# Kernel tuning notes

Hardware: AMD Instinct MI355X
Metric: run time of the kernel (lower is better)

## Reference

```python
import jax, jax.numpy as jnp
import numpy as np

WS = 7          # window_size
NH = 4          # num_heads
C = 128         # channels
N = WS * WS     # tokens per window = 49
BW = 4096       # number of windows total (batch * windows_per_image)
NW = 64         # windows per image (mask leading dim)


def _rel_pos_index(ws):
    coords = np.stack(np.meshgrid(np.arange(ws), np.arange(ws), indexing='ij'))
    cf = coords.reshape(2, -1)
    rel = (cf[:, :, None] - cf[:, None, :]).transpose(1, 2, 0)
    rel[:, :, 0] += ws - 1
    rel[:, :, 1] += ws - 1
    rel[:, :, 0] *= 2 * ws - 1
    return jnp.asarray(rel.sum(-1).ravel(), dtype=jnp.int32)  # [N*N]


def setup_inputs() -> dict:
    key = jax.random.key(0)
    ks = jax.random.split(key, 6)
    x = jax.random.normal(ks[0], (BW, N, C), dtype=jnp.float32)
    qkv_w = jax.random.normal(ks[1], (C, 3 * C), dtype=jnp.float32) * 0.02
    qkv_b = jnp.zeros((3 * C,), dtype=jnp.float32)
    proj_w = jax.random.normal(ks[2], (C, C), dtype=jnp.float32) * 0.02
    proj_b = jnp.zeros((C,), dtype=jnp.float32)
    bias_table = jax.random.normal(ks[3], ((2 * WS - 1) ** 2, NH), dtype=jnp.float32) * 0.02
    # Swin shifted-window mask: 0 where attention allowed, -100 where blocked
    keep = jax.random.bernoulli(ks[4], 0.5, (NW, N, N))
    mask = jnp.where(keep, 0.0, -100.0).astype(jnp.float32)
    return {"x": x, "qkv_w": qkv_w, "qkv_b": qkv_b, "proj_w": proj_w,
            "proj_b": proj_b, "bias_table": bias_table, "mask": mask}


def reference(x, qkv_w, qkv_b, proj_w, proj_b, bias_table, mask):
    B_, n, c = x.shape
    h = NH
    d = c // h
    scale = d ** -0.5

    qkv = x @ qkv_w + qkv_b                       # [B_, N, 3C]
    qkv = qkv.reshape(B_, n, 3, h, d).transpose(2, 0, 3, 1, 4)  # [3, B_, h, N, d]
    q, k, v = qkv[0], qkv[1], qkv[2]

    attn = jnp.einsum('bhnd,bhmd->bhnm', q * scale, k)          # [B_, h, N, N]

    idx = _rel_pos_index(WS)
    rpb = bias_table[idx].reshape(n, n, h).transpose(2, 0, 1)   # [h, N, N]
    attn = attn + rpb[None]

    nW = mask.shape[0]
    attn = attn.reshape(-1, nW, h, n, n) + mask[None, :, None]  # [B, nW, h, N, N]
    attn = attn.reshape(-1, h, n, n)
    attn = jax.nn.softmax(attn, axis=-1)

    out = jnp.einsum('bhnm,bhmd->bhnd', attn, v)  # [B_, h, N, d]
    out = out.transpose(0, 2, 1, 3).reshape(B_, n, c)
    return out @ proj_w + proj_b
```

## Files before the change

### kernel.cpp

```cpp
#include <hip/hip_runtime.h>

#define NTOK 49
#define CH   128
#define NHEAD 4
#define SCALE 0.17677669529663687f

typedef __bf16 bf16x8 __attribute__((ext_vector_type(8)));
typedef short  s16x8  __attribute__((ext_vector_type(8)));
typedef float  f32x4  __attribute__((ext_vector_type(4)));

__device__ __forceinline__ unsigned short f2bf(float f) {
  unsigned int u = __builtin_bit_cast(unsigned int, f);
  u += 0x7FFFu + ((u >> 16) & 1u);
  return (unsigned short)(u >> 16);
}

__device__ __forceinline__ f32x4 mfma_bf16(s16x8 a, s16x8 b, f32x4 c) {
  return __builtin_amdgcn_mfma_f32_16x16x32_bf16(
      __builtin_bit_cast(bf16x8, a), __builtin_bit_cast(bf16x8, b), c, 0, 0, 0);
}

__global__ void prep_kernel(const float* __restrict__ qkv_w,
                            const float* __restrict__ proj_w,
                            const float* __restrict__ bias_table,
                            unsigned short* __restrict__ wT,
                            unsigned short* __restrict__ pT,
                            float* __restrict__ rpb) {
  int t = blockIdx.x * 256 + threadIdx.x;
  if (t < 384 * 128) {
    int n = t >> 7, k = t & 127;
    float v = qkv_w[k * 384 + n];
    if (n < 128) v *= SCALE;
    wT[n * 128 + k] = f2bf(v);
  } else if (t < 384 * 128 + 128 * 128) {
    int u = t - 384 * 128;
    int n = u >> 7, k = u & 127;
    pT[n * 128 + k] = f2bf(proj_w[k * 128 + n]);
  } else if (t < 384 * 128 + 128 * 128 + NHEAD * NTOK * NTOK) {
    int u = t - (384 * 128 + 128 * 128);
    int h = u / (NTOK * NTOK);
    int ij = u % (NTOK * NTOK);
    int i = ij / NTOK, j = ij % NTOK;
    int idx = (i / 7 - j / 7 + 6) * 13 + (i % 7 - j % 7 + 6);
    rpb[h * (NTOK * NTOK) + ij] = bias_table[idx * NHEAD + h];
  }
}

__global__ __launch_bounds__(256, 2)
void attn_fused_kernel(const float* __restrict__ x,
                       const float* __restrict__ qkv_b,
                       const float* __restrict__ proj_b,
                       const float* __restrict__ mask,
                       const unsigned short* __restrict__ wT,
                       const unsigned short* __restrict__ pT,
                       const float* __restrict__ rpb,
                       float* __restrict__ out) {
  __shared__ __align__(16) char smem_raw[76800];
  unsigned short* const Xs     = (unsigned short*)smem_raw;
  unsigned short* const QKbase = (unsigned short*)(smem_raw + 17408);
  unsigned short* const VTbase = (unsigned short*)(smem_raw + 58368);

  const int w    = blockIdx.x;
  const int tid  = threadIdx.x;
  const int wave = tid >> 6;
  const int lane = tid & 63;
  const int quad = lane >> 4;
  const int l16  = lane & 15;
  const int h    = wave;

  unsigned short* const qs = QKbase + wave * 5120;
  unsigned short* const ks = qs + 2560;
  unsigned short* const ps = QKbase + wave * 5120;
  unsigned short* const vt = VTbase + wave * 2304;

  const f32x4 fzero = {0.f, 0.f, 0.f, 0.f};

  {
    const float* xw = x + (size_t)w * (NTOK * CH);
    for (int t = tid; t < NTOK * 32; t += 256) {
      const int row = t >> 5;
      const int c4  = (t & 31) << 2;
      const float4 v = *(const float4*)(xw + row * CH + c4);
      ushort4 pk;
      pk.x = f2bf(v.x); pk.y = f2bf(v.y); pk.z = f2bf(v.z); pk.w = f2bf(v.w);
      *(ushort4*)(Xs + row * 136 + c4) = pk;
    }
    for (int t = tid; t < 15 * 32; t += 256) {
      const int row = 49 + (t >> 5);
      const int c4  = (t & 31) << 2;
      ushort4 z; z.x = 0; z.y = 0; z.z = 0; z.w = 0;
      *(ushort4*)(Xs + row * 136 + c4) = z;
    }
  }
  __syncthreads();

#pragma unroll
  for (int part = 0; part < 3; ++part) {
    f32x4 acc[4][2];
#pragma unroll
    for (int mt = 0; mt < 4; ++mt)
#pragma unroll
      for (int nt = 0; nt < 2; ++nt) acc[mt][nt] = fzero;
    const int nbase = part * 128 + h * 32;
#pragma unroll
    for (int kt = 0; kt < 4; ++kt) {
      s16x8 a[4], b[2];
#pragma unroll
      for (int mt = 0; mt < 4; ++mt)
        a[mt] = *(const s16x8*)(Xs + (mt * 16 + l16) * 136 + kt * 32 + quad * 8);
#pragma unroll
      for (int nt = 0; nt < 2; ++nt)
        b[nt] = *(const s16x8*)(wT + (size_t)(nbase + nt * 16 + l16) * 128 + kt * 32 + quad * 8);
#pragma unroll
      for (int mt = 0; mt < 4; ++mt)
#pragma unroll
        for (int nt = 0; nt < 2; ++nt)
          acc[mt][nt] = mfma_bf16(a[mt], b[nt], acc[mt][nt]);
    }
#pragma unroll
    for (int nt = 0; nt < 2; ++nt) {
      float bias = qkv_b[nbase + nt * 16 + l16];
      if (part == 0) bias *= SCALE;
#pragma unroll
      for (int mt = 0; mt < 4; ++mt)
#pragma unroll
        for (int r = 0; r < 4; ++r) {
          const int row = mt * 16 + quad * 4 + r;
          const int col = nt * 16 + l16;
          const unsigned short bv = f2bf(acc[mt][nt][r] + bias);
          if (part == 0)      qs[row * 40 + col] = bv;
          else if (part == 1) ks[row * 40 + col] = bv;
          else                vt[col * 72 + row] = bv;
        }
    }
  }
  __syncthreads();

  s16x8 qf[4], kf[4];
#pragma unroll
  for (int mt = 0; mt < 4; ++mt)
    qf[mt] = *(const s16x8*)(qs + (mt * 16 + l16) * 40 + quad * 8);
#pragma unroll
  for (int nt = 0; nt < 4; ++nt)
    kf[nt] = *(const s16x8*)(ks + (nt * 16 + l16) * 40 + quad * 8);
  f32x4 s[4][4];
#pragma unroll
  for (int mt = 0; mt < 4; ++mt)
#pragma unroll
    for (int nt = 0; nt < 4; ++nt)
      s[mt][nt] = mfma_bf16(qf[mt], kf[nt], fzero);

  const float* maskw = mask + (size_t)(w & 63) * (NTOK * NTOK);
  const float* rpbh  = rpb + h * (NTOK * NTOK);
  float rinv[4][4];
#pragma unroll
  for (int mt = 0; mt < 4; ++mt) {
#pragma unroll
    for (int r = 0; r < 4; ++r) {
      const int i = mt * 16 + quad * 4 + r;
      float vals[4];
      float vmax = -1e30f;
#pragma unroll
      for (int nt = 0; nt < 4; ++nt) {
        const int j = nt * 16 + l16;
        float v = -1e30f;
        if (i < NTOK && j < NTOK) {
          const int ij = i * NTOK + j;
          v = s[mt][nt][r] + rpbh[ij] + maskw[ij];
        }
        vals[nt] = v;
        vmax = fmaxf(vmax, v);
      }
#pragma unroll
      for (int off = 1; off < 16; off <<= 1)
        vmax = fmaxf(vmax, __shfl_xor(vmax, off, 64));
      float rsum = 0.f;
#pragma unroll
      for (int nt = 0; nt < 4; ++nt) {
        const float e = __expf(vals[nt] - vmax);
        vals[nt] = e;
        rsum += e;
      }
#pragma unroll
      for (int off = 1; off < 16; off <<= 1)
        rsum += __shfl_xor(rsum, off, 64);
      rinv[mt][r] = 1.f / rsum;
#pragma unroll
      for (int nt = 0; nt < 4; ++nt)
        ps[i * 72 + nt * 16 + l16] = f2bf(vals[nt]);
    }
  }

  f32x4 o[4][2];
#pragma unroll
  for (int mt = 0; mt < 4; ++mt)
#pragma unroll
    for (int nt = 0; nt < 2; ++nt) o[mt][nt] = fzero;
#pragma unroll
  for (int kt = 0; kt < 2; ++kt) {
    s16x8 pf[4], vf[2];
#pragma unroll
    for (int mt = 0; mt < 4; ++mt)
      pf[mt] = *(const s16x8*)(ps + (mt * 16 + l16) * 72 + kt * 32 + quad * 8);
#pragma unroll
    for (int nt = 0; nt < 2; ++nt)
      vf[nt] = *(const s16x8*)(vt + (nt * 16 + l16) * 72 + kt * 32 + quad * 8);
#pragma unroll
    for (int mt = 0; mt < 4; ++mt)
#pragma unroll
      for (int nt = 0; nt < 2; ++nt)
        o[mt][nt] = mfma_bf16(pf[mt], vf[nt], o[mt][nt]);
  }

  unsigned short* const ao = Xs;
#pragma unroll
  for (int mt = 0; mt < 4; ++mt)
#pragma unroll
    for (int nt = 0; nt < 2; ++nt)
#pragma unroll
      for (int r = 0; r < 4; ++r) {
        const int row = mt * 16 + quad * 4 + r;
        const int col = h * 32 + nt * 16 + l16;
        ao[row * 136 + col] = f2bf(o[mt][nt][r] * rinv[mt][r]);
      }
  __syncthreads();

  f32x4 po[4][2];
#pragma unroll
  for (int mt = 0; mt < 4; ++mt)
#pragma unroll
    for (int nt = 0; nt < 2; ++nt) po[mt][nt] = fzero;
#pragma unroll
  for (int kt = 0; kt < 4; ++kt) {
    s16x8 a[4], b[2];
#pragma unroll
    for (int mt = 0; mt < 4; ++mt)
      a[mt] = *(const s16x8*)(ao + (mt * 16 + l16) * 136 + kt * 32 + quad * 8);
#pragma unroll
    for (int nt = 0; nt < 2; ++nt)
      b[nt] = *(const s16x8*)(pT + (size_t)(h * 32 + nt * 16 + l16) * 128 + kt * 32 + quad * 8);
#pragma unroll
    for (int mt = 0; mt < 4; ++mt)
#pragma unroll
      for (int nt = 0; nt < 2; ++nt)
        po[mt][nt] = mfma_bf16(a[mt], b[nt], po[mt][nt]);
  }
  float* outw = out + (size_t)w * (NTOK * CH);
#pragma unroll
  for (int nt = 0; nt < 2; ++nt) {
    const int col = h * 32 + nt * 16 + l16;
    const float pb = proj_b[col];
#pragma unroll
    for (int mt = 0; mt < 4; ++mt)
#pragma unroll
      for (int r = 0; r < 4; ++r) {
        const int row = mt * 16 + quad * 4 + r;
        if (row < NTOK) outw[row * CH + col] = po[mt][nt][r] + pb;
      }
  }
}

extern "C" void kernel_launch(void* const* d_in, const int* in_sizes, int n_in,
                              void* d_out, int out_size, void* d_ws, size_t ws_size,
                              hipStream_t stream) {
  (void)in_sizes; (void)n_in; (void)out_size; (void)ws_size;
  const float* x          = (const float*)d_in[0];
  const float* qkv_w      = (const float*)d_in[1];
  const float* qkv_b      = (const float*)d_in[2];
  const float* proj_w     = (const float*)d_in[3];
  const float* proj_b     = (const float*)d_in[4];
  const float* bias_table = (const float*)d_in[5];
  const float* mask       = (const float*)d_in[6];
  float* out = (float*)d_out;

  unsigned short* wT = (unsigned short*)d_ws;
  unsigned short* pT = wT + 384 * 128;
  float* rpb = (float*)(pT + 128 * 128);

  const int prep_items = 384 * 128 + 128 * 128 + NHEAD * NTOK * NTOK;
  prep_kernel<<<(prep_items + 255) / 256, 256, 0, stream>>>(qkv_w, proj_w, bias_table,
                                                            wT, pT, rpb);
  attn_fused_kernel<<<4096, 256, 0, stream>>>(x, qkv_b, proj_b, mask, wT, pT, rpb, out);
}
```

Before: 319.7 us.

## Split window rows across eight waves and compute softmax sums with MFMA

Doubles the block to 512 threads so each head's rows are split across two waves. This halves per-wave MFMA and register work and raises waves per CU under the fixed LDS budget. Softmax drops the max-subtraction and shuffle reductions: it stores exp(logit) directly and gets row sums with an MFMA against a ones vector. The prep kernel now reads weights coalesced. The risk is that unshifted exp can overflow for large logits, and an extra barrier is needed because P overwrites the Q/K buffers.

```diff
diff --git a/kernel.cpp b/kernel.cpp
--- a/kernel.cpp
+++ b/kernel.cpp
@@ -28,14 +28,14 @@
                             float* __restrict__ rpb) {
   int t = blockIdx.x * 256 + threadIdx.x;
   if (t < 384 * 128) {
-    int n = t >> 7, k = t & 127;
-    float v = qkv_w[k * 384 + n];
+    int k = t / 384, n = t % 384;
+    float v = qkv_w[t];
     if (n < 128) v *= SCALE;
     wT[n * 128 + k] = f2bf(v);
   } else if (t < 384 * 128 + 128 * 128) {
     int u = t - 384 * 128;
-    int n = u >> 7, k = u & 127;
-    pT[n * 128 + k] = f2bf(proj_w[k * 128 + n]);
+    int k = u >> 7, n = u & 127;
+    pT[n * 128 + k] = f2bf(proj_w[u]);
   } else if (t < 384 * 128 + 128 * 128 + NHEAD * NTOK * NTOK) {
     int u = t - (384 * 128 + 128 * 128);
     int h = u / (NTOK * NTOK);
@@ -46,7 +46,7 @@
   }
 }
 
-__global__ __launch_bounds__(256, 2)
+__global__ __launch_bounds__(512, 4)
 void attn_fused_kernel(const float* __restrict__ x,
                        const float* __restrict__ qkv_b,
                        const float* __restrict__ proj_b,
@@ -56,28 +56,30 @@
                        const float* __restrict__ rpb,
                        float* __restrict__ out) {
   __shared__ __align__(16) char smem_raw[76800];
-  unsigned short* const Xs     = (unsigned short*)smem_raw;
-  unsigned short* const QKbase = (unsigned short*)(smem_raw + 17408);
-  unsigned short* const VTbase = (unsigned short*)(smem_raw + 58368);
+  unsigned short* const Xs = (unsigned short*)smem_raw;
+  unsigned short* const QK = (unsigned short*)(smem_raw + 17408);
+  unsigned short* const VT = (unsigned short*)(smem_raw + 58368);
 
   const int w    = blockIdx.x;
   const int tid  = threadIdx.x;
-  const int wave = tid >> 6;
+  const int wv   = tid >> 6;
+  const int h    = wv & 3;
+  const int mh   = wv >> 2;
   const int lane = tid & 63;
   const int quad = lane >> 4;
   const int l16  = lane & 15;
-  const int h    = wave;
-
-  unsigned short* const qs = QKbase + wave * 5120;
+  const int rowbase = mh * 32;
+
+  unsigned short* const qs = QK + h * 5120;
   unsigned short* const ks = qs + 2560;
-  unsigned short* const ps = QKbase + wave * 5120;
-  unsigned short* const vt = VTbase + wave * 2304;
+  unsigned short* const ps = QK + h * 5120;
+  unsigned short* const vt = VT + h * 2304;
 
   const f32x4 fzero = {0.f, 0.f, 0.f, 0.f};
 
   {
     const float* xw = x + (size_t)w * (NTOK * CH);
-    for (int t = tid; t < NTOK * 32; t += 256) {
+    for (int t = tid; t < NTOK * 32; t += 512) {
       const int row = t >> 5;
       const int c4  = (t & 31) << 2;
       const float4 v = *(const float4*)(xw + row * CH + c4);
@@ -85,7 +87,7 @@
       pk.x = f2bf(v.x); pk.y = f2bf(v.y); pk.z = f2bf(v.z); pk.w = f2bf(v.w);
       *(ushort4*)(Xs + row * 136 + c4) = pk;
     }
-    for (int t = tid; t < 15 * 32; t += 256) {
+    for (int t = tid; t < 15 * 32; t += 512) {
       const int row = 49 + (t >> 5);
       const int c4  = (t & 31) << 2;
       ushort4 z; z.x = 0; z.y = 0; z.z = 0; z.w = 0;
@@ -94,72 +96,76 @@
   }
   __syncthreads();
 
-#pragma unroll
-  for (int part = 0; part < 3; ++part) {
-    f32x4 acc[4][2];
-#pragma unroll
-    for (int mt = 0; mt < 4; ++mt)
-#pragma unroll
-      for (int nt = 0; nt < 2; ++nt) acc[mt][nt] = fzero;
-    const int nbase = part * 128 + h * 32;
-#pragma unroll
-    for (int kt = 0; kt < 4; ++kt) {
-      s16x8 a[4], b[2];
-#pragma unroll
-      for (int mt = 0; mt < 4; ++mt)
-        a[mt] = *(const s16x8*)(Xs + (mt * 16 + l16) * 136 + kt * 32 + quad * 8);
-#pragma unroll
-      for (int nt = 0; nt < 2; ++nt)
-        b[nt] = *(const s16x8*)(wT + (size_t)(nbase + nt * 16 + l16) * 128 + kt * 32 + quad * 8);
-#pragma unroll
-      for (int mt = 0; mt < 4; ++mt)
+  f32x4 acc[3][2][2];
+#pragma unroll
+  for (int p = 0; p < 3; ++p)
+#pragma unroll
+    for (int mt = 0; mt < 2; ++mt)
+#pragma unroll
+      for (int nt = 0; nt < 2; ++nt) acc[p][mt][nt] = fzero;
+
+#pragma unroll
+  for (int kt = 0; kt < 4; ++kt) {
+    s16x8 a[2];
+#pragma unroll
+    for (int mt = 0; mt < 2; ++mt)
+      a[mt] = *(const s16x8*)(Xs + (rowbase + mt * 16 + l16) * 136 + kt * 32 + quad * 8);
+#pragma unroll
+    for (int p = 0; p < 3; ++p) {
+      s16x8 b[2];
+#pragma unroll
+      for (int nt = 0; nt < 2; ++nt)
+        b[nt] = *(const s16x8*)(wT + (size_t)(p * 128 + h * 32 + nt * 16 + l16) * 128 +
+                                kt * 32 + quad * 8);
+#pragma unroll
+      for (int mt = 0; mt < 2; ++mt)
 #pragma unroll
         for (int nt = 0; nt < 2; ++nt)
-          acc[mt][nt] = mfma_bf16(a[mt], b[nt], acc[mt][nt]);
-    }
+          acc[p][mt][nt] = mfma_bf16(a[mt], b[nt], acc[p][mt][nt]);
+    }
+  }
+#pragma unroll
+  for (int p = 0; p < 3; ++p)
 #pragma unroll
     for (int nt = 0; nt < 2; ++nt) {
-      float bias = qkv_b[nbase + nt * 16 + l16];
-      if (part == 0) bias *= SCALE;
-#pragma unroll
-      for (int mt = 0; mt < 4; ++mt)
+      const int col = nt * 16 + l16;
+      float bias = qkv_b[p * 128 + h * 32 + col];
+      if (p == 0) bias *= SCALE;
+#pragma unroll
+      for (int mt = 0; mt < 2; ++mt)
 #pragma unroll
         for (int r = 0; r < 4; ++r) {
-          const int row = mt * 16 + quad * 4 + r;
-          const int col = nt * 16 + l16;
-          const unsigned short bv = f2bf(acc[mt][nt][r] + bias);
-          if (part == 0)      qs[row * 40 + col] = bv;
-          else if (part == 1) ks[row * 40 + col] = bv;
-          else                vt[col * 72 + row] = bv;
+          const int row = rowbase + mt * 16 + quad * 4 + r;
+          const unsigned short bv = f2bf(acc[p][mt][nt][r] + bias);
+          if (p == 0)      qs[row * 40 + col] = bv;
+          else if (p == 1) ks[row * 40 + col] = bv;
+          else             vt[col * 72 + row] = bv;
         }
     }
-  }
-  __syncthreads();
-
-  s16x8 qf[4], kf[4];
-#pragma unroll
-  for (int mt = 0; mt < 4; ++mt)
-    qf[mt] = *(const s16x8*)(qs + (mt * 16 + l16) * 40 + quad * 8);
+  __syncthreads();
+
+  s16x8 qf[2], kf[4];
+#pragma unroll
+  for (int mt = 0; mt < 2; ++mt)
+    qf[mt] = *(const s16x8*)(qs + (rowbase + mt * 16 + l16) * 40 + quad * 8);
 #pragma unroll
   for (int nt = 0; nt < 4; ++nt)
     kf[nt] = *(const s16x8*)(ks + (nt * 16 + l16) * 40 + quad * 8);
-  f32x4 s[4][4];
-#pragma unroll
-  for (int mt = 0; mt < 4; ++mt)
+  f32x4 s[2][4];
+#pragma unroll
+  for (int mt = 0; mt < 2; ++mt)
 #pragma unroll
     for (int nt = 0; nt < 4; ++nt)
       s[mt][nt] = mfma_bf16(qf[mt], kf[nt], fzero);
+  __syncthreads();
 
   const float* maskw = mask + (size_t)(w & 63) * (NTOK * NTOK);
   const float* rpbh  = rpb + h * (NTOK * NTOK);
-  float rinv[4][4];
-#pragma unroll
-  for (int mt = 0; mt < 4; ++mt) {
+#pragma unroll
+  for (int mt = 0; mt < 2; ++mt)
 #pragma unroll
     for (int r = 0; r < 4; ++r) {
-      const int i = mt * 16 + quad * 4 + r;
-      float vals[4];
-      float vmax = -1e30f;
+      const int i = rowbase + mt * 16 + quad * 4 + r;
 #pragma unroll
       for (int nt = 0; nt < 4; ++nt) {
         const int j = nt * 16 + l16;
@@ -168,79 +174,71 @@
           const int ij = i * NTOK + j;
           v = s[mt][nt][r] + rpbh[ij] + maskw[ij];
         }
-        vals[nt] = v;
-        vmax = fmaxf(vmax, v);
+        ps[i * 72 + j] = f2bf(__expf(v));
       }
-#pragma unroll
-      for (int off = 1; off < 16; off <<= 1)
-        vmax = fmaxf(vmax, __shfl_xor(vmax, off, 64));
-      float rsum = 0.f;
-#pragma unroll
-      for (int nt = 0; nt < 4; ++nt) {
-        const float e = __expf(vals[nt] - vmax);
-        vals[nt] = e;
-        rsum += e;
-      }
-#pragma unroll
-      for (int off = 1; off < 16; off <<= 1)
-        rsum += __shfl_xor(rsum, off, 64);
-      rinv[mt][r] = 1.f / rsum;
-#pragma unroll
-      for (int nt = 0; nt < 4; ++nt)
-        ps[i * 72 + nt * 16 + l16] = f2bf(vals[nt]);
-    }
-  }
-
-  f32x4 o[4][2];
-#pragma unroll
-  for (int mt = 0; mt < 4; ++mt)
+    }
+
+  s16x8 pf[2][2], vf[2][2], ones;
+#pragma unroll
+  for (int e = 0; e < 8; ++e) ones[e] = (short)0x3F80;
+#pragma unroll
+  for (int mt = 0; mt < 2; ++mt)
+#pragma unroll
+    for (int kt = 0; kt < 2; ++kt)
+      pf[mt][kt] = *(const s16x8*)(ps + (rowbase + mt * 16 + l16) * 72 + kt * 32 + quad * 8);
+#pragma unroll
+  for (int nt = 0; nt < 2; ++nt)
+#pragma unroll
+    for (int kt = 0; kt < 2; ++kt)
+      vf[nt][kt] = *(const s16x8*)(vt + (nt * 16 + l16) * 72 + kt * 32 + quad * 8);
+
+  f32x4 o[2][2], rs[2];
+#pragma unroll
+  for (int mt = 0; mt < 2; ++mt) {
+    rs[mt] = fzero;
 #pragma unroll
     for (int nt = 0; nt < 2; ++nt) o[mt][nt] = fzero;
-#pragma unroll
-  for (int kt = 0; kt < 2; ++kt) {
-    s16x8 pf[4], vf[2];
-#pragma unroll
-    for (int mt = 0; mt < 4; ++mt)
-      pf[mt] = *(const s16x8*)(ps + (mt * 16 + l16) * 72 + kt * 32 + quad * 8);
-#pragma unroll
-    for (int nt = 0; nt < 2; ++nt)
-      vf[nt] = *(const s16x8*)(vt + (nt * 16 + l16) * 72 + kt * 32 + quad * 8);
-#pragma unroll
-    for (int mt = 0; mt < 4; ++mt)
-#pragma unroll
-      for (int nt = 0; nt < 2; ++nt)
-        o[mt][nt] = mfma_bf16(pf[mt], vf[nt], o[mt][nt]);
-  }
+  }
+#pragma unroll
+  for (int kt = 0; kt < 2; ++kt)
+#pragma unroll
+    for (int mt = 0; mt < 2; ++mt) {
+      rs[mt] = mfma_bf16(pf[mt][kt], ones, rs[mt]);
+#pragma unroll
+      for (int nt = 0; nt < 2; ++nt)
+        o[mt][nt] = mfma_bf16(pf[mt][kt], vf[nt][kt], o[mt][nt]);
+    }
 
   unsigned short* const ao = Xs;
 #pragma unroll
-  for (int mt = 0; mt < 4; ++mt)
-#pragma unroll
-    for (int nt = 0; nt < 2; ++nt)
-#pragma unroll
-      for (int r = 0; r < 4; ++r) {
-        const int row = mt * 16 + quad * 4 + r;
-        const int col = h * 32 + nt * 16 + l16;
-        ao[row * 136 + col] = f2bf(o[mt][nt][r] * rinv[mt][r]);
-      }
-  __syncthreads();
-
-  f32x4 po[4][2];
-#pragma unroll
-  for (int mt = 0; mt < 4; ++mt)
+  for (int mt = 0; mt < 2; ++mt)
+#pragma unroll
+    for (int r = 0; r < 4; ++r) {
+      const float rsv  = rs[mt][r];
+      const float rinv = rsv > 0.f ? 1.f / rsv : 0.f;
+      const int row = rowbase + mt * 16 + quad * 4 + r;
+#pragma unroll
+      for (int nt = 0; nt < 2; ++nt)
+        ao[row * 136 + h * 32 + nt * 16 + l16] = f2bf(o[mt][nt][r] * rinv);
+    }
+  __syncthreads();
+
+  f32x4 po[2][2];
+#pragma unroll
+  for (int mt = 0; mt < 2; ++mt)
 #pragma unroll
     for (int nt = 0; nt < 2; ++nt) po[mt][nt] = fzero;
 #pragma unroll
   for (int kt = 0; kt < 4; ++kt) {
-    s16x8 a[4], b[2];
-#pragma unroll
-    for (int mt = 0; mt < 4; ++mt)
-      a[mt] = *(const s16x8*)(ao + (mt * 16 + l16) * 136 + kt * 32 + quad * 8);
+    s16x8 a[2], b[2];
+#pragma unroll
+    for (int mt = 0; mt < 2; ++mt)
+      a[mt] = *(const s16x8*)(ao + (rowbase + mt * 16 + l16) * 136 + kt * 32 + quad * 8);
 #pragma unroll
     for (int nt = 0; nt < 2; ++nt)
       b[nt] = *(const s16x8*)(pT + (size_t)(h * 32 + nt * 16 + l16) * 128 + kt * 32 + quad * 8);
 #pragma unroll
-    for (int mt = 0; mt < 4; ++mt)
+    for (int mt = 0; mt < 2; ++mt)
 #pragma unroll
       for (int nt = 0; nt < 2; ++nt)
         po[mt][nt] = mfma_bf16(a[mt], b[nt], po[mt][nt]);
@@ -251,10 +249,10 @@
     const int col = h * 32 + nt * 16 + l16;
     const float pb = proj_b[col];
 #pragma unroll
-    for (int mt = 0; mt < 4; ++mt)
+    for (int mt = 0; mt < 2; ++mt)
 #pragma unroll
       for (int r = 0; r < 4; ++r) {
-        const int row = mt * 16 + quad * 4 + r;
+        const int row = rowbase + mt * 16 + quad * 4 + r;
         if (row < NTOK) outw[row * CH + col] = po[mt][nt][r] + pb;
       }
   }
@@ -280,5 +278,5 @@
   const int prep_items = 384 * 128 + 128 * 128 + NHEAD * NTOK * NTOK;
   prep_kernel<<<(prep_items + 255) / 256, 256, 0, stream>>>(qkv_w, proj_w, bias_table,
                                                             wT, pT, rpb);
-  attn_fused_kernel<<<4096, 256, 0, stream>>>(x, qkv_b, proj_b, mask, wT, pT, rpb, out);
-}
+  attn_fused_kernel<<<4096, 512, 0, stream>>>(x, qkv_b, proj_b, mask, wT, pT, rpb, out);
+}
```

Result: slower. 379.5 us (+18.7%).
